# Optimization experiments

Measured on AMD Instinct MI355X. Metric: run time of the kernel, lower is better.

Reference implementation:

```python
import jax, jax.numpy as jnp
import numpy as np

B = 256
DIM = 2048
H = W = 8
SLICE_MAX = 64
SLICE_RANGE = 2
TEMP = 0.1
BN_EPS = 1e-5
COS_EPS = 1e-8


def setup_inputs() -> dict:
    key = jax.random.key(0)
    ks = jax.random.split(key, 6)
    z0 = jax.random.normal(ks[0], (B, DIM, H, W), dtype=jnp.float32)
    z1 = jax.random.normal(ks[1], (B, DIM, H, W), dtype=jnp.float32)
    rel0 = jax.random.randint(ks[2], (B,), 0, SLICE_MAX)
    rel1 = jax.random.randint(ks[3], (B,), 0, SLICE_MAX)
    W1 = jax.random.normal(ks[4], (DIM, DIM), dtype=jnp.float32) * 0.02
    W2 = jax.random.normal(ks[5], (DIM, DIM), dtype=jnp.float32) * 0.02
    return {
        "z0": z0, "z1": z1,
        "rel_slice_idx_0": rel0, "rel_slice_idx_1": rel1,
        "W1": W1, "b1": jnp.zeros((DIM,), jnp.float32),
        "gamma": jnp.ones((DIM,), jnp.float32), "beta": jnp.zeros((DIM,), jnp.float32),
        "W2": W2, "b2": jnp.zeros((DIM,), jnp.float32),
    }


def _projection_head(z, W1, b1, gamma, beta, W2, b2):
    # AdaptiveAvgPool2d(1) + Flatten: [N, C, H, W] -> [N, C]
    p = jnp.mean(z, axis=(2, 3))
    h = p @ W1.T + b1
    # BatchNorm1d in training mode: batch statistics (biased variance)
    mu = jnp.mean(h, axis=0)
    var = jnp.var(h, axis=0)
    h = (h - mu) * jax.lax.rsqrt(var + BN_EPS) * gamma + beta
    h = jax.nn.relu(h)
    return h @ W2.T + b2


def reference(z0, z1, rel_slice_idx_0, rel_slice_idx_1, W1, b1, gamma, beta, W2, b2):
    # domain_contrast=True -> rel_slice_idx = rel_slice_idx_0 only
    rel = rel_slice_idx_0
    z = jnp.concatenate([z0, z1], axis=0)           # [2B, C, H, W]
    z = _projection_head(z, W1, b1, gamma, beta, W2, b2)  # [2B, DIM]

    # full cosine-similarity matrix (fused, instead of the per-row python loop)
    norms = jnp.maximum(jnp.linalg.norm(z, axis=1, keepdims=True), COS_EPS)
    zn = z / norms
    sim = zn @ zn.T                                  # [2B, 2B]
    # similarity_weighting='none' -> weights == 1
    S = jnp.exp(sim / TEMP)

    # relative-position pos/neg masks over the first B (same-domain) samples
    diff = jnp.abs(rel[:, None] - rel[None, :])      # [B, B]
    eye = jnp.eye(B, dtype=bool)
    pos_mask = (diff <= SLICE_RANGE) & (~eye)
    neg_mask = diff > SLICE_RANGE

    S_bb = S[:B, :B]
    # negatives = same-domain negatives + ALL other-domain samples (domain_contrast)
    neg_sum = jnp.sum(S_bb * neg_mask, axis=1) + jnp.sum(S[:B, B:], axis=1)  # [B]

    terms = -jnp.log(S_bb / (S_bb + neg_sum[:, None]))  # [B, B]
    cnt = jnp.sum(pos_mask, axis=1)
    loss_b = jnp.sum(terms * pos_mask, axis=1) / jnp.maximum(cnt, 1)
    defined = cnt > 0
    loss = jnp.sum(jnp.where(defined, loss_b, 0.0))
    n_defined = jnp.sum(defined)
    return loss, n_defined
```

## Files before the change

kernel.cpp:

```cpp
#include <hip/hip_runtime.h>

typedef __attribute__((ext_vector_type(8))) short s8v;
typedef __attribute__((ext_vector_type(4))) short s4v;
typedef __attribute__((ext_vector_type(4))) float f4v;

#define DIM 2048
#define NROW 512
#define NB 256

__device__ inline short f2bf(float f) {
    union { float f; unsigned int u; } v; v.f = f;
    unsigned int u = v.u;
    unsigned int r = (u + 0x7fffu + ((u >> 16) & 1u)) >> 16;
    return (short)r;
}

__device__ __forceinline__ int pk_trunc(float a, float b) {
    return __builtin_amdgcn_perm(__float_as_uint(b), __float_as_uint(a), 0x07060302);
}

__device__ __forceinline__ float qsum(float s) {
    int i = __float_as_int(s);
    s += __int_as_float(__builtin_amdgcn_update_dpp(i, i, 0xB1, 0xF, 0xF, false));
    i = __float_as_int(s);
    s += __int_as_float(__builtin_amdgcn_update_dpp(i, i, 0x4E, 0xF, 0xF, false));
    return s;
}

__global__ __launch_bounds__(256) void pool_cast(const float* __restrict__ z0,
                                                 const float* __restrict__ z1,
                                                 const float* __restrict__ W1,
                                                 const float* __restrict__ W2,
                                                 short* __restrict__ p,
                                                 short* __restrict__ w1h,
                                                 short* __restrict__ w2h,
                                                 float* __restrict__ stats) {
    int t = threadIdx.x;
    int c = blockIdx.x;
    if (c < 8192) {
        const float* src = (c < 4096) ? z0 + (long)c * 8192 : z1 + (long)(c - 4096) * 8192;
        int g = t >> 2, sub = t & 3;
        const float* base = src + g * 128 + sub * 4;
        f4v v[8];
#pragma unroll
        for (int j = 0; j < 8; ++j) v[j] = __builtin_nontemporal_load((const f4v*)(base + j * 16));
        __builtin_amdgcn_sched_barrier(0);
        float sA = 0.f, sB = 0.f;
#pragma unroll
        for (int j = 0; j < 4; ++j) sA += v[j].x + v[j].y + v[j].z + v[j].w;
#pragma unroll
        for (int j = 4; j < 8; ++j) sB += v[j].x + v[j].y + v[j].z + v[j].w;
        sA = qsum(sA);
        sB = qsum(sB);
        if (sub == 0) {
            int pk = (int)(unsigned short)f2bf(sA * (1.0f / 64.0f))
                   | ((int)(unsigned short)f2bf(sB * (1.0f / 64.0f)) << 16);
            ((int*)p)[c * 64 + g] = pk;
        }
    } else {
        int cc = c - 8192;
        const float* w = (cc < 2048) ? W1 : W2;
        short* o = (cc < 2048) ? w1h : w2h;
        int idx = (cc & 2047) * 2048 + t * 8;
        f4v x = __builtin_nontemporal_load((const f4v*)(w + idx));
        f4v y = __builtin_nontemporal_load((const f4v*)(w + idx + 4));
        int4 o4;
        o4.x = pk_trunc(x.x, x.y);
        o4.y = pk_trunc(x.z, x.w);
        o4.z = pk_trunc(y.x, y.y);
        o4.w = pk_trunc(y.z, y.w);
        *(int4*)(o + idx) = o4;
        if (cc == 0) {
#pragma unroll
            for (int k = 0; k < 16; ++k) stats[t + k * 256] = 0.f;
        }
    }
}

__device__ __forceinline__ int swz(int r, int k) { return r * 256 + (k ^ ((r & 7) << 3)); }

__global__ __launch_bounds__(256) void gemm_ks(const short* __restrict__ A,
                                               const short* __restrict__ Bh,
                                               const float* __restrict__ Bf,
                                               const float* __restrict__ bias,
                                               float* __restrict__ C,
                                               float* __restrict__ stats,
                                               int M, int N, int K, int kChunk) {
    __shared__ short sm[2 * 64 * 256];
    short* lA = sm;
    short* lB = sm + 64 * 256;
    int t = threadIdx.x;
    int n0 = blockIdx.x * 64, m0 = blockIdx.y * 64;
    int kbase = blockIdx.z * kChunk;
    long zoff = (long)blockIdx.z * M * N;
    int lane = t & 63, w = t >> 6;
    int l16 = lane & 15, quad = lane >> 4;
    int ks = w * 64;
    f4v acc[4][4] = {};
    int sr = t >> 3;
    int sq8 = (t & 7) * 8;

    for (int it = 0; it < kChunk; it += 256) {
        int k0 = kbase + it;
#pragma unroll
        for (int pp = 0; pp < 2; ++pp) {
            int r = sr + pp * 32;
            const short* as = &A[(long)(m0 + r) * K + k0];
#pragma unroll
            for (int j = 0; j < 4; ++j)
                *(s8v*)&lA[swz(r, sq8 + j * 64)] = *(const s8v*)&as[sq8 + j * 64];
        }
        if (Bh) {
#pragma unroll
            for (int pp = 0; pp < 2; ++pp) {
                int r = sr + pp * 32;
                const short* bs = &Bh[(long)(n0 + r) * K + k0];
#pragma unroll
                for (int j = 0; j < 4; ++j)
                    *(s8v*)&lB[swz(r, sq8 + j * 64)] = *(const s8v*)&bs[sq8 + j * 64];
            }
        } else {
#pragma unroll
            for (int pp = 0; pp < 2; ++pp) {
                int r = sr + pp * 32;
                const float* bs = &Bf[(long)(n0 + r) * K + k0];
#pragma unroll
                for (int j = 0; j < 4; ++j) {
                    float4 x = *(const float4*)&bs[sq8 + j * 64];
                    float4 y = *(const float4*)&bs[sq8 + j * 64 + 4];
                    int4 o;
                    o.x = pk_trunc(x.x, x.y);
                    o.y = pk_trunc(x.z, x.w);
                    o.z = pk_trunc(y.x, y.y);
                    o.w = pk_trunc(y.z, y.w);
                    *(int4*)&lB[swz(r, sq8 + j * 64)] = o;
                }
            }
        }
        __syncthreads();
#pragma unroll
        for (int kk = 0; kk < 2; ++kk) {
            s8v af[4], bf[4];
#pragma unroll
            for (int i = 0; i < 4; ++i)
                af[i] = *(const s8v*)&lA[swz(i * 16 + l16, ks + kk * 32 + quad * 8)];
#pragma unroll
            for (int j = 0; j < 4; ++j)
                bf[j] = *(const s8v*)&lB[swz(j * 16 + l16, ks + kk * 32 + quad * 8)];
#pragma unroll
            for (int i = 0; i < 4; ++i)
#pragma unroll
                for (int j = 0; j < 4; ++j)
                    acc[i][j] = __builtin_amdgcn_mfma_f32_16x16x32_bf16(af[i], bf[j], acc[i][j], 0, 0, 0);
        }
        __syncthreads();
    }

    float* fr = (float*)sm;
#pragma unroll
    for (int i = 0; i < 4; ++i)
#pragma unroll
        for (int j = 0; j < 4; ++j)
#pragma unroll
            for (int r = 0; r < 4; ++r)
                fr[w * 4096 + (i * 16 + quad * 4 + r) * 64 + j * 16 + l16] = acc[i][j][r];
    __syncthreads();
    int c = t & 63;
    int rbase = (t >> 6) * 16;
    float bv = bias ? bias[n0 + c] : 0.0f;
    float s = 0.f, q = 0.f;
#pragma unroll
    for (int r = 0; r < 16; ++r) {
        int rr = rbase + r;
        float h = fr[rr * 64 + c] + fr[4096 + rr * 64 + c]
                + fr[8192 + rr * 64 + c] + fr[12288 + rr * 64 + c] + bv;
        C[zoff + (long)(m0 + rr) * N + n0 + c] = h;
        s += h; q += h * h;
    }
    if (stats) {
        __syncthreads();
        fr[(t >> 6) * 64 + c] = s;
        fr[256 + (t >> 6) * 64 + c] = q;
        __syncthreads();
        if (t < 64) {
            float ss = fr[t] + fr[64 + t] + fr[128 + t] + fr[192 + t];
            float qq = fr[256 + t] + fr[320 + t] + fr[384 + t] + fr[448 + t];
            atomicAdd(&stats[n0 + t], ss);
            atomicAdd(&stats[2048 + n0 + t], qq);
        }
    }
}

__global__ __launch_bounds__(256) void bn_relu_cast(const float* __restrict__ h,
                                                    const float* __restrict__ stats,
                                                    const float* __restrict__ gamma,
                                                    const float* __restrict__ beta,
                                                    short* __restrict__ hn) {
    int idx = (blockIdx.x * 256 + threadIdx.x) * 4;
    int col = idx & (DIM - 1);
    float4 s0 = *(const float4*)(stats + col);
    float4 s1 = *(const float4*)(stats + 2048 + col);
    float4 g  = *(const float4*)(gamma + col);
    float4 bt = *(const float4*)(beta + col);
    float4 v  = *(const float4*)(h + idx);
    float mu, var, sc, sh;
    s4v o;
    mu = s0.x * (1.0f / NROW); var = s1.x * (1.0f / NROW) - mu * mu;
    sc = g.x * rsqrtf(var + 1e-5f); sh = bt.x - mu * sc;
    o.x = f2bf(fmaxf(v.x * sc + sh, 0.f));
    mu = s0.y * (1.0f / NROW); var = s1.y * (1.0f / NROW) - mu * mu;
    sc = g.y * rsqrtf(var + 1e-5f); sh = bt.y - mu * sc;
    o.y = f2bf(fmaxf(v.y * sc + sh, 0.f));
    mu = s0.z * (1.0f / NROW); var = s1.z * (1.0f / NROW) - mu * mu;
    sc = g.z * rsqrtf(var + 1e-5f); sh = bt.z - mu * sc;
    o.z = f2bf(fmaxf(v.z * sc + sh, 0.f));
    mu = s0.w * (1.0f / NROW); var = s1.w * (1.0f / NROW) - mu * mu;
    sc = g.w * rsqrtf(var + 1e-5f); sh = bt.w - mu * sc;
    o.w = f2bf(fmaxf(v.w * sc + sh, 0.f));
    *(s4v*)(hn + idx) = o;
}

__global__ __launch_bounds__(256) void rownorm(const float* __restrict__ z,
                                               short* __restrict__ zn,
                                               float* __restrict__ out) {
    __shared__ float red[4];
    int row = blockIdx.x, t = threadIdx.x;
    if (row == 0 && t == 0) { out[0] = 0.f; out[1] = 0.f; }
    const float* zr = z + (long)row * DIM;
    float4 v0 = *(const float4*)(zr + t * 4);
    float4 v1 = *(const float4*)(zr + 1024 + t * 4);
    float ss = v0.x * v0.x + v0.y * v0.y + v0.z * v0.z + v0.w * v0.w
             + v1.x * v1.x + v1.y * v1.y + v1.z * v1.z + v1.w * v1.w;
#pragma unroll
    for (int m = 1; m < 64; m <<= 1) ss += __shfl_xor(ss, m);
    if ((t & 63) == 0) red[t >> 6] = ss;
    __syncthreads();
    float tot = red[0] + red[1] + red[2] + red[3];
    float inv = 1.0f / fmaxf(sqrtf(tot), 1e-8f);
    s4v a, b;
    a.x = f2bf(v0.x * inv); a.y = f2bf(v0.y * inv); a.z = f2bf(v0.z * inv); a.w = f2bf(v0.w * inv);
    b.x = f2bf(v1.x * inv); b.y = f2bf(v1.y * inv); b.z = f2bf(v1.z * inv); b.w = f2bf(v1.w * inv);
    *(s4v*)(zn + (long)row * DIM + t * 4) = a;
    *(s4v*)(zn + (long)row * DIM + 1024 + t * 4) = b;
}

__global__ __launch_bounds__(256) void loss_fused(const float* __restrict__ simp,
                                                  const int* __restrict__ rel,
                                                  float* __restrict__ out) {
    __shared__ float red[4], rts[4], rct[4];
    int i = blockIdx.x, t = threadIdx.x, lane = t & 63, wave = t >> 6;
    int reli = rel[i];
    float s0 = 0.f, s1 = 0.f;
#pragma unroll
    for (int z = 0; z < 8; ++z) {
        s0 += simp[(long)z * 131072 + i * 512 + t];
        s1 += simp[(long)z * 131072 + i * 512 + 256 + t];
    }
    float e0 = __expf(10.0f * s0);
    float e1 = __expf(10.0f * s1);
    int d = abs(reli - rel[t]);
    float neg = e1 + ((d > 2) ? e0 : 0.f);
#pragma unroll
    for (int m = 1; m < 64; m <<= 1) neg += __shfl_xor(neg, m);
    if (lane == 0) red[wave] = neg;
    __syncthreads();
    neg = red[0] + red[1] + red[2] + red[3];
    float ts = 0.f, cnt = 0.f;
    if (t != i && d <= 2) { ts = logf(e0 + neg) - 10.0f * s0; cnt = 1.f; }
#pragma unroll
    for (int m = 1; m < 64; m <<= 1) { ts += __shfl_xor(ts, m); cnt += __shfl_xor(cnt, m); }
    if (lane == 0) { rts[wave] = ts; rct[wave] = cnt; }
    __syncthreads();
    if (t == 0) {
        float T = rts[0] + rts[1] + rts[2] + rts[3];
        float C = rct[0] + rct[1] + rct[2] + rct[3];
        atomicAdd(&out[0], C > 0.f ? T / C : 0.f);
        atomicAdd(&out[1], C > 0.f ? 1.f : 0.f);
    }
}

extern "C" void kernel_launch(void* const* d_in, const int* in_sizes, int n_in,
                              void* d_out, int out_size, void* d_ws, size_t ws_size,
                              hipStream_t stream) {
    const float* z0    = (const float*)d_in[0];
    const float* z1    = (const float*)d_in[1];
    const int*   rel0  = (const int*)d_in[2];
    const float* W1    = (const float*)d_in[4];
    const float* b1    = (const float*)d_in[5];
    const float* gamma = (const float*)d_in[6];
    const float* beta  = (const float*)d_in[7];
    const float* W2    = (const float*)d_in[8];
    const float* b2    = (const float*)d_in[9];

    char* ws = (char*)d_ws;
    short* p_bf  = (short*)(ws);
    float* h     = (float*)(ws + (2l  << 20));
    short* hn    = (short*)(ws + (6l  << 20));
    float* zproj = (float*)(ws + (8l  << 20));
    short* zn    = (short*)(ws + (12l << 20));
    float* simp  = (float*)(ws + (14l << 20));
    float* stats = (float*)(ws + (19l << 20));
    short* w1h   = (short*)(ws + (20l << 20));
    short* w2h   = (short*)(ws + (28l << 20));
    bool castok = ws_size >= (36l << 20);

    if (castok) {
        pool_cast<<<12288, 256, 0, stream>>>(z0, z1, W1, W2, p_bf, w1h, w2h, stats);
    } else {
        hipMemsetAsync(stats, 0, 16384, stream);
        pool_cast<<<8192, 256, 0, stream>>>(z0, z1, nullptr, nullptr, p_bf,
                                            nullptr, nullptr, nullptr);
    }
    gemm_ks<<<dim3(32, 8, 1), 256, 0, stream>>>(p_bf, castok ? w1h : nullptr,
                                                castok ? nullptr : W1, b1, h, stats,
                                                NROW, DIM, DIM, DIM);
    bn_relu_cast<<<1024, 256, 0, stream>>>(h, stats, gamma, beta, hn);
    gemm_ks<<<dim3(32, 8, 1), 256, 0, stream>>>(hn, castok ? w2h : nullptr,
                                                castok ? nullptr : W2, b2, zproj, nullptr,
                                                NROW, DIM, DIM, DIM);
    rownorm<<<512, 256, 0, stream>>>(zproj, zn, (float*)d_out);
    gemm_ks<<<dim3(8, 4, 8), 256, 0, stream>>>(zn, zn, nullptr, nullptr, simp, nullptr,
                                               NB, NROW, DIM, 256);
    loss_fused<<<NB, 256, 0, stream>>>(simp, rel0, (float*)d_out);
}
```

Baseline: 337.1 us.

## Add double-buffered register-prefetch GEMM kernel for bf16 cast path

```diff
diff --git a/kernel.cpp b/kernel.cpp
--- a/kernel.cpp
+++ b/kernel.cpp
@@ -78,6 +78,110 @@
 }
 
 __device__ __forceinline__ int swz(int r, int k) { return r * 256 + (k ^ ((r & 7) << 3)); }
+__device__ __forceinline__ int swz2(int r, int k) { return r * 128 + (k ^ ((r & 7) << 3)); }
+
+__global__ __launch_bounds__(256, 1) void gemm_db(const short* __restrict__ A,
+                                                  const short* __restrict__ B,
+                                                  const float* __restrict__ bias,
+                                                  float* __restrict__ C,
+                                                  float* __restrict__ stats,
+                                                  int M, int N, int K, int kChunk) {
+    __shared__ short sm[2][16384];
+    int t = threadIdx.x;
+    int n0 = blockIdx.x * 64, m0 = blockIdx.y * 64;
+    int kbase = blockIdx.z * kChunk;
+    long zoff = (long)blockIdx.z * M * N;
+    int lane = t & 63, w = t >> 6;
+    int l16 = lane & 15, quad = lane >> 4;
+    int ks = w * 32;
+    f4v acc[4][4] = {};
+    int srow = t >> 4;
+    int skoff = (t & 15) * 8;
+    const short* aBase = &A[(long)(m0 + srow) * K + skoff];
+    const short* bBase = &B[(long)(n0 + srow) * K + skoff];
+    long rstride = (long)16 * K;
+    int nIter = kChunk >> 7;
+    s8v ra[4], rb[4];
+
+#pragma unroll
+    for (int pp = 0; pp < 4; ++pp) ra[pp] = *(const s8v*)(aBase + pp * rstride + kbase);
+#pragma unroll
+    for (int pp = 0; pp < 4; ++pp) rb[pp] = *(const s8v*)(bBase + pp * rstride + kbase);
+#pragma unroll
+    for (int pp = 0; pp < 4; ++pp) *(s8v*)&sm[0][swz2(srow + pp * 16, skoff)] = ra[pp];
+#pragma unroll
+    for (int pp = 0; pp < 4; ++pp) *(s8v*)&sm[0][8192 + swz2(srow + pp * 16, skoff)] = rb[pp];
+    __syncthreads();
+
+    for (int it = 0; it < nIter; ++it) {
+        int cur = it & 1;
+        bool pf = (it + 1) < nIter;
+        if (pf) {
+            int k0 = kbase + (it + 1) * 128;
+#pragma unroll
+            for (int pp = 0; pp < 4; ++pp) ra[pp] = *(const s8v*)(aBase + pp * rstride + k0);
+#pragma unroll
+            for (int pp = 0; pp < 4; ++pp) rb[pp] = *(const s8v*)(bBase + pp * rstride + k0);
+        }
+        __builtin_amdgcn_sched_barrier(0);
+        const short* lA = sm[cur];
+        const short* lB = sm[cur] + 8192;
+        s8v af[4], bf[4];
+#pragma unroll
+        for (int i = 0; i < 4; ++i)
+            af[i] = *(const s8v*)&lA[swz2(i * 16 + l16, ks + quad * 8)];
+#pragma unroll
+        for (int j = 0; j < 4; ++j)
+            bf[j] = *(const s8v*)&lB[swz2(j * 16 + l16, ks + quad * 8)];
+#pragma unroll
+        for (int i = 0; i < 4; ++i)
+#pragma unroll
+            for (int j = 0; j < 4; ++j)
+                acc[i][j] = __builtin_amdgcn_mfma_f32_16x16x32_bf16(af[i], bf[j], acc[i][j], 0, 0, 0);
+        if (pf) {
+            int nb = cur ^ 1;
+#pragma unroll
+            for (int pp = 0; pp < 4; ++pp) *(s8v*)&sm[nb][swz2(srow + pp * 16, skoff)] = ra[pp];
+#pragma unroll
+            for (int pp = 0; pp < 4; ++pp) *(s8v*)&sm[nb][8192 + swz2(srow + pp * 16, skoff)] = rb[pp];
+        }
+        __syncthreads();
+    }
+
+    float* fr = (float*)sm;
+#pragma unroll
+    for (int i = 0; i < 4; ++i)
+#pragma unroll
+        for (int j = 0; j < 4; ++j)
+#pragma unroll
+            for (int r = 0; r < 4; ++r)
+                fr[w * 4096 + (i * 16 + quad * 4 + r) * 64 + j * 16 + l16] = acc[i][j][r];
+    __syncthreads();
+    int c = t & 63;
+    int rbase = (t >> 6) * 16;
+    float bv = bias ? bias[n0 + c] : 0.0f;
+    float s = 0.f, q = 0.f;
+#pragma unroll
+    for (int r = 0; r < 16; ++r) {
+        int rr = rbase + r;
+        float h = fr[rr * 64 + c] + fr[4096 + rr * 64 + c]
+                + fr[8192 + rr * 64 + c] + fr[12288 + rr * 64 + c] + bv;
+        C[zoff + (long)(m0 + rr) * N + n0 + c] = h;
+        s += h; q += h * h;
+    }
+    if (stats) {
+        __syncthreads();
+        fr[(t >> 6) * 64 + c] = s;
+        fr[256 + (t >> 6) * 64 + c] = q;
+        __syncthreads();
+        if (t < 64) {
+            float ss = fr[t] + fr[64 + t] + fr[128 + t] + fr[192 + t];
+            float qq = fr[256 + t] + fr[320 + t] + fr[384 + t] + fr[448 + t];
+            atomicAdd(&stats[n0 + t], ss);
+            atomicAdd(&stats[2048 + n0 + t], qq);
+        }
+    }
+}
 
 __global__ __launch_bounds__(256) void gemm_ks(const short* __restrict__ A,
                                                const short* __restrict__ Bh,
@@ -306,20 +410,27 @@
 
     if (castok) {
         pool_cast<<<12288, 256, 0, stream>>>(z0, z1, W1, W2, p_bf, w1h, w2h, stats);
+        gemm_db<<<dim3(32, 8, 1), 256, 0, stream>>>(p_bf, w1h, b1, h, stats,
+                                                    NROW, DIM, DIM, DIM);
+        bn_relu_cast<<<1024, 256, 0, stream>>>(h, stats, gamma, beta, hn);
+        gemm_db<<<dim3(32, 8, 1), 256, 0, stream>>>(hn, w2h, b2, zproj, nullptr,
+                                                    NROW, DIM, DIM, DIM);
+        rownorm<<<512, 256, 0, stream>>>(zproj, zn, (float*)d_out);
+        gemm_db<<<dim3(8, 4, 8), 256, 0, stream>>>(zn, zn, nullptr, simp, nullptr,
+                                                   NB, NROW, DIM, 256);
+        loss_fused<<<NB, 256, 0, stream>>>(simp, rel0, (float*)d_out);
     } else {
         hipMemsetAsync(stats, 0, 16384, stream);
         pool_cast<<<8192, 256, 0, stream>>>(z0, z1, nullptr, nullptr, p_bf,
                                             nullptr, nullptr, nullptr);
-    }
-    gemm_ks<<<dim3(32, 8, 1), 256, 0, stream>>>(p_bf, castok ? w1h : nullptr,
-                                                castok ? nullptr : W1, b1, h, stats,
-                                                NROW, DIM, DIM, DIM);
-    bn_relu_cast<<<1024, 256, 0, stream>>>(h, stats, gamma, beta, hn);
-    gemm_ks<<<dim3(32, 8, 1), 256, 0, stream>>>(hn, castok ? w2h : nullptr,
-                                                castok ? nullptr : W2, b2, zproj, nullptr,
-                                                NROW, DIM, DIM, DIM);
-    rownorm<<<512, 256, 0, stream>>>(zproj, zn, (float*)d_out);
-    gemm_ks<<<dim3(8, 4, 8), 256, 0, stream>>>(zn, zn, nullptr, nullptr, simp, nullptr,
-                                               NB, NROW, DIM, 256);
-    loss_fused<<<NB, 256, 0, stream>>>(simp, rel0, (float*)d_out);
-}
+        gemm_ks<<<dim3(32, 8, 1), 256, 0, stream>>>(p_bf, nullptr, W1, b1, h, stats,
+                                                    NROW, DIM, DIM, DIM);
+        bn_relu_cast<<<1024, 256, 0, stream>>>(h, stats, gamma, beta, hn);
+        gemm_ks<<<dim3(32, 8, 1), 256, 0, stream>>>(hn, nullptr, W2, b2, zproj, nullptr,
+                                                    NROW, DIM, DIM, DIM);
+        rownorm<<<512, 256, 0, stream>>>(zproj, zn, (float*)d_out);
+        gemm_ks<<<dim3(8, 4, 8), 256, 0, stream>>>(zn, zn, nullptr, nullptr, simp, nullptr,
+                                                   NB, NROW, DIM, 256);
+        loss_fused<<<NB, 256, 0, stream>>>(simp, rel0, (float*)d_out);
+    }
+}
```

New measurement: 331.0 us. No clear change (-1.8%).
